# Kernel optimization log

Measured on AMD Instinct MI355X. Metric: run time of the kernel, lower is better.

## Reference

```python
import jax, jax.numpy as jnp
import numpy as np

NEG_BIG = -9e15


def gat_layer(h, adj, W, a, alpha, concat):
    # h: (N, Fin), W: (Fin, Fout), a: (2*Fout, 1)
    Wh = h @ W                                   # (N, Fout)
    F = Wh.shape[1]
    # e[i,j] = LeakyReLU(cat(Wh_i, Wh_j) @ a) = LeakyReLU(s_i + d_j)
    s = Wh @ a[:F, 0]                            # (N,)
    d = Wh @ a[F:, 0]                            # (N,)
    e = jax.nn.leaky_relu(s[:, None] + d[None, :], negative_slope=alpha)  # (N, N)
    e = jnp.where(adj > 0, e, NEG_BIG)
    att = jax.nn.softmax(e, axis=1)              # (N, N)
    out = att @ Wh                               # (N, Fout)
    return jax.nn.elu(out) if concat else out


def setup_inputs() -> dict:
    key = jax.random.key(0)
    ks = jax.random.split(key, 12)
    N, nfeat, nhid, nlatent, nclass = 8192, 512, 256, 64, 16

    def xavier(k, shape):
        gain = 1.414
        fan_in, fan_out = shape[0], shape[1]
        bound = gain * np.sqrt(6.0 / (fan_in + fan_out))
        return jax.random.uniform(k, shape, jnp.float32, -bound, bound)

    x = jax.random.normal(ks[0], (N, nfeat), jnp.float32)
    adj = jax.random.randint(ks[1], (N, N), 0, 2, jnp.int32)
    eps = jax.random.normal(ks[2], (N, nlatent), jnp.float32)
    return {
        "x": x,
        "adj": adj,
        "eps": eps,
        "W1": xavier(ks[3], (nfeat, nhid)),
        "a1": xavier(ks[4], (2 * nhid, 1)),
        "Wmu": xavier(ks[5], (nhid, nlatent)),
        "amu": xavier(ks[6], (2 * nlatent, 1)),
        "Wlv": xavier(ks[7], (nhid, nlatent)),
        "alv": xavier(ks[8], (2 * nlatent, 1)),
        "Wc": xavier(ks[9], (nlatent, nclass)),
        "bc": jnp.zeros((nclass,), jnp.float32),
    }


def reference(x, adj, eps, W1, a1, Wmu, amu, Wlv, alv, Wc, bc):
    alpha = 0.2  # LeakyReLU negative slope
    # eval mode: all dropouts are identity
    h = gat_layer(x, adj, W1, a1, alpha, concat=True)      # (N, nhid)
    mu = gat_layer(h, adj, Wmu, amu, alpha, concat=False)  # (N, nlatent)
    logvar = gat_layer(h, adj, Wlv, alv, alpha, concat=False)
    z = mu + eps * jnp.exp(0.5 * logvar)
    logits = z @ Wc + bc                                   # (N, nclass)
    return logits, mu, logvar
```

## Files before the change

kernel.cpp:

```cpp
#include <hip/hip_runtime.h>

typedef unsigned short u16;
typedef __attribute__((ext_vector_type(8))) short short8;
typedef __attribute__((ext_vector_type(4))) float f32x4;

#define NROW 8192

__device__ __forceinline__ float bf2f(u16 h) {
  unsigned u = ((unsigned)h) << 16;
  return __builtin_bit_cast(float, u);
}
__device__ __forceinline__ float ldf(const void* p, size_t i, int f32) {
  return f32 ? ((const float*)p)[i] : bf2f(((const u16*)p)[i]);
}
__device__ __forceinline__ u16 f2bf(float f) {
  unsigned b = __builtin_bit_cast(unsigned, f);
  b += 0x7FFFu + ((b >> 16) & 1u);
  return (u16)(b >> 16);
}

__global__ void detect3(const u16* __restrict__ xr, unsigned* __restrict__ mode) {
  __shared__ int zc, bg;
  int t = threadIdx.x;
  if (t == 0) { zc = 0; bg = 0; }
  __syncthreads();
  int zeros_even = 0; int big = 0;
  for (int i = t; i < 4096; i += 256) {
    u16 v = xr[i];
    if (!(i & 1) && v == 0) zeros_even++;
    if (fabsf(bf2f(v)) > 1e6f) big = 1;
  }
  atomicAdd(&zc, zeros_even);
  if (big) atomicOr(&bg, 1);
  __syncthreads();
  if (t == 0) *mode = (zc > 512 || bg) ? 1u : 0u;
}

__global__ void detect_adj(const unsigned* __restrict__ a, unsigned* __restrict__ amode) {
  __shared__ int clo;
  int t = threadIdx.x;
  if (t == 0) clo = 0;
  __syncthreads();
  int c = 0;
  for (int i = t; i < 4096; i += 256)
    if (a[i] == 0x00003F80u) c++;
  atomicAdd(&clo, c);
  __syncthreads();
  if (t == 0) *amode = (clo > 32) ? 1u : 0u;
}

struct AdjRaw { int4 w0, w1; };
__device__ __forceinline__ AdjRaw adj_load(const void* adj, size_t base, int amode) {
  AdjRaw r;
  if (amode == 0) {
    const int4* p = (const int4*)((const int*)adj + base);
    r.w0 = p[0]; r.w1 = p[1];
  } else {
    r.w0 = *(const int4*)((const u16*)adj + base);
    r.w1 = make_int4(0, 0, 0, 0);
  }
  return r;
}
__device__ __forceinline__ void adj_decode(const AdjRaw& r, int amode, int* aa) {
  if (amode == 0) {
    aa[0] = r.w0.x != 0; aa[1] = r.w0.y != 0; aa[2] = r.w0.z != 0; aa[3] = r.w0.w != 0;
    aa[4] = r.w1.x != 0; aa[5] = r.w1.y != 0; aa[6] = r.w1.z != 0; aa[7] = r.w1.w != 0;
  } else {
    aa[0] = (r.w0.x & 0xFFFF) != 0; aa[1] = ((unsigned)r.w0.x >> 16) != 0;
    aa[2] = (r.w0.y & 0xFFFF) != 0; aa[3] = ((unsigned)r.w0.y >> 16) != 0;
    aa[4] = (r.w0.z & 0xFFFF) != 0; aa[5] = ((unsigned)r.w0.z >> 16) != 0;
    aa[6] = (r.w0.w & 0xFFFF) != 0; aa[7] = ((unsigned)r.w0.w >> 16) != 0;
  }
}

__global__ __launch_bounds__(256) void gemm_mfma(const u16* __restrict__ Abf,
    const u16* __restrict__ BT, float* __restrict__ C, int K, int N) {
  int tid = threadIdx.x;
  int l = tid & 63, w = tid >> 6;
  int m0 = blockIdx.y * 64, n0 = blockIdx.x * 64;
  const u16* arow = Abf + (size_t)(m0 + w * 16 + (l & 15)) * K + (l >> 4) * 8;
  const u16* brow = BT + (size_t)(n0 + (l & 15)) * K + (l >> 4) * 8;
  f32x4 acc[4];
#pragma unroll
  for (int nt = 0; nt < 4; ++nt) acc[nt] = (f32x4){0.f, 0.f, 0.f, 0.f};
  for (int k0 = 0; k0 < K; k0 += 32) {
    short8 a = *(const short8*)(arow + k0);
#pragma unroll
    for (int nt = 0; nt < 4; ++nt) {
      short8 b = *(const short8*)(brow + (size_t)nt * 16 * K + k0);
      acc[nt] = __builtin_amdgcn_mfma_f32_16x16x32_bf16(a, b, acc[nt], 0, 0, 0);
    }
  }
#pragma unroll
  for (int nt = 0; nt < 4; ++nt)
#pragma unroll
    for (int q = 0; q < 4; ++q)
      C[(size_t)(m0 + w * 16 + (l >> 4) * 4 + q) * N + n0 + nt * 16 + (l & 15)] =
          acc[nt][q];
}

__global__ __launch_bounds__(256) void gemm2_dual(const u16* __restrict__ Abf,
    const u16* __restrict__ BT0, const u16* __restrict__ BT1,
    float* __restrict__ C0, float* __restrict__ C1) {
  const int K = 256, N = 64;
  const u16* BT = blockIdx.x ? BT1 : BT0;
  float* C = blockIdx.x ? C1 : C0;
  int tid = threadIdx.x, l = tid & 63, w = tid >> 6;
  int m0 = blockIdx.y * 64;
  const u16* arow = Abf + (size_t)(m0 + w * 16 + (l & 15)) * K + (l >> 4) * 8;
  const u16* brow = BT + (size_t)(l & 15) * K + (l >> 4) * 8;
  f32x4 acc[4];
#pragma unroll
  for (int nt = 0; nt < 4; ++nt) acc[nt] = (f32x4){0.f, 0.f, 0.f, 0.f};
  for (int k0 = 0; k0 < K; k0 += 32) {
    short8 a = *(const short8*)(arow + k0);
#pragma unroll
    for (int nt = 0; nt < 4; ++nt) {
      short8 b = *(const short8*)(brow + (size_t)nt * 16 * K + k0);
      acc[nt] = __builtin_amdgcn_mfma_f32_16x16x32_bf16(a, b, acc[nt], 0, 0, 0);
    }
  }
#pragma unroll
  for (int nt = 0; nt < 4; ++nt)
#pragma unroll
    for (int q = 0; q < 4; ++q)
      C[(size_t)(m0 + w * 16 + (l >> 4) * 4 + q) * N + nt * 16 + (l & 15)] = acc[nt][q];
}

__global__ __launch_bounds__(256) void convert_bf16(const void* __restrict__ in,
    u16* __restrict__ out, int n8, const unsigned* __restrict__ modep) {
  int f32 = (int)*modep;
  int i = blockIdx.x * 256 + threadIdx.x;
  if (i >= n8) return;
  if (f32) {
    float4 v0 = ((const float4*)in)[(size_t)i * 2];
    float4 v1 = ((const float4*)in)[(size_t)i * 2 + 1];
    ushort4 o0 = {f2bf(v0.x), f2bf(v0.y), f2bf(v0.z), f2bf(v0.w)};
    ushort4 o1 = {f2bf(v1.x), f2bf(v1.y), f2bf(v1.z), f2bf(v1.w)};
    ((ushort4*)out)[(size_t)i * 2] = o0;
    ((ushort4*)out)[(size_t)i * 2 + 1] = o1;
  } else {
    ((int4*)out)[i] = ((const int4*)in)[i];
  }
}

__global__ __launch_bounds__(256) void transpose_bf16(const float* __restrict__ in,
    u16* __restrict__ out, int M, int F) {
  __shared__ float t[32][33];
  int m0 = blockIdx.x * 32, f0 = blockIdx.y * 32;
  int c = threadIdx.x & 31, r = threadIdx.x >> 5;
  for (int rr = r; rr < 32; rr += 8)
    t[rr][c] = in[(size_t)(m0 + rr) * F + f0 + c];
  __syncthreads();
  for (int rr = r; rr < 32; rr += 8)
    out[(size_t)(f0 + rr) * M + m0 + c] = f2bf(t[c][rr]);
}

__global__ __launch_bounds__(256) void transpose_pair(const float* __restrict__ in0,
    const float* __restrict__ in1, u16* __restrict__ out0, u16* __restrict__ out1,
    int M, int F) {
  const float* in = blockIdx.z ? in1 : in0;
  u16* out = blockIdx.z ? out1 : out0;
  __shared__ float t[32][33];
  int m0 = blockIdx.x * 32, f0 = blockIdx.y * 32;
  int c = threadIdx.x & 31, r = threadIdx.x >> 5;
  for (int rr = r; rr < 32; rr += 8)
    t[rr][c] = in[(size_t)(m0 + rr) * F + f0 + c];
  __syncthreads();
  for (int rr = r; rr < 32; rr += 8)
    out[(size_t)(f0 + rr) * M + m0 + c] = f2bf(t[c][rr]);
}

__global__ __launch_bounds__(256) void transpose_any(const void* __restrict__ in,
    u16* __restrict__ out, int M, int F, const unsigned* __restrict__ modep) {
  int f32 = (int)*modep;
  __shared__ u16 t[32][33];
  int m0 = blockIdx.x * 32, f0 = blockIdx.y * 32;
  int c = threadIdx.x & 31, r = threadIdx.x >> 5;
  for (int rr = r; rr < 32; rr += 8)
    t[rr][c] = f2bf(ldf(in, (size_t)(m0 + rr) * F + f0 + c, f32));
  __syncthreads();
  for (int rr = r; rr < 32; rr += 8)
    out[(size_t)(f0 + rr) * M + m0 + c] = t[c][rr];
}

__global__ __launch_bounds__(256) void transpose_w2(const void* __restrict__ in0,
    const void* __restrict__ in1, u16* __restrict__ out0, u16* __restrict__ out1,
    int M, int F, const unsigned* __restrict__ modep) {
  int f32 = (int)*modep;
  const void* in = blockIdx.z ? in1 : in0;
  u16* out = blockIdx.z ? out1 : out0;
  __shared__ u16 t[32][33];
  int m0 = blockIdx.x * 32, f0 = blockIdx.y * 32;
  int c = threadIdx.x & 31, r = threadIdx.x >> 5;
  for (int rr = r; rr < 32; rr += 8)
    t[rr][c] = f2bf(ldf(in, (size_t)(m0 + rr) * F + f0 + c, f32));
  __syncthreads();
  for (int rr = r; rr < 32; rr += 8)
    out[(size_t)(f0 + rr) * M + m0 + c] = t[c][rr];
}

__global__ __launch_bounds__(256) void sd_f32(const float* __restrict__ Wh,
    const void* __restrict__ a2, float* __restrict__ s, float* __restrict__ d,
    int F, const unsigned* __restrict__ modep) {
  int f32 = (int)*modep;
  int row = blockIdx.x * 4 + (threadIdx.x >> 6);
  int l = threadIdx.x & 63;
  float ss = 0.f, dd = 0.f;
  for (int k = l; k < F; k += 64) {
    float wv = Wh[(size_t)row * F + k];
    ss += wv * ldf(a2, k, f32);
    dd += wv * ldf(a2, F + k, f32);
  }
#pragma unroll
  for (int off = 32; off > 0; off >>= 1) {
    ss += __shfl_down(ss, off, 64);
    dd += __shfl_down(dd, off, 64);
  }
  if (l == 0) { s[row] = ss; d[row] = dd; }
}

__global__ __launch_bounds__(256) void sd_dual(const float* __restrict__ Wh0,
    const float* __restrict__ Wh1, const void* __restrict__ a0,
    const void* __restrict__ a1, float* __restrict__ s0, float* __restrict__ s1,
    float* __restrict__ d0, float* __restrict__ d1,
    const unsigned* __restrict__ modep) {
  int f32 = (int)*modep;
  int L = blockIdx.y;
  const float* Wh = L ? Wh1 : Wh0;
  const void* a2 = L ? a1 : a0;
  int row = blockIdx.x * 4 + (threadIdx.x >> 6);
  int l = threadIdx.x & 63;
  float wv = Wh[(size_t)row * 64 + l];
  float ss = wv * ldf(a2, l, f32);
  float dd = wv * ldf(a2, 64 + l, f32);
#pragma unroll
  for (int off = 32; off > 0; off >>= 1) {
    ss += __shfl_down(ss, off, 64);
    dd += __shfl_down(dd, off, 64);
  }
  if (l == 0) { (L ? s1 : s0)[row] = ss; (L ? d1 : d0)[row] = dd; }
}

__global__ __launch_bounds__(256) void dmax_reduce(const float* __restrict__ da,
    const float* __restrict__ db, float* __restrict__ cells) {
  const float* d = blockIdx.x ? db : da;
  __shared__ float red[256];
  float m = -3.4e38f;
  for (int i = threadIdx.x; i < NROW; i += 256) m = fmaxf(m, d[i]);
  red[threadIdx.x] = m;
  __syncthreads();
#pragma unroll
  for (int sft = 128; sft > 0; sft >>= 1) {
    if (threadIdx.x < sft) red[threadIdx.x] = fmaxf(red[threadIdx.x], red[threadIdx.x + sft]);
    __syncthreads();
  }
  if (threadIdx.x == 0) cells[blockIdx.x * 16] = red[0];
}

__device__ __forceinline__ int pa_off(int L, int s, int mh, int row, int kg) {
  return ((L * 4 + s * 2 + mh) << 10) + (row << 6) + ((kg ^ ((row >> 1) & 3)) << 4);
}

template <int NL, int FDIM, int JS>
__global__ __launch_bounds__(256) void flash_mfma(
    const u16* __restrict__ whTa, const u16* __restrict__ whTb,
    const float* __restrict__ sa, const float* __restrict__ da,
    const float* __restrict__ sb, const float* __restrict__ db,
    const float* __restrict__ cella, const float* __restrict__ cellb,
    const void* __restrict__ adj, const unsigned* __restrict__ amodep,
    float* __restrict__ acca, float* __restrict__ lsa,
    float* __restrict__ accb, float* __restrict__ lsb) {
  constexpr int JLEN = NROW / JS;
  constexpr int NIT = JLEN / 64;
  constexpr int NTW = (NL == 1) ? 4 : 2;
  constexpr int NRBLK = NROW / 32;
  __shared__ __align__(16) char PA[2][NL * 4096];
  __shared__ __align__(16) float dd_[NL][JLEN];
  __shared__ float sv_[NL][32], Ms_[NL][32];
  int tid = threadIdx.x;
  int amode = (int)*amodep;
  int rblk = blockIdx.x % NRBLK, js = blockIdx.x / NRBLK;
  int r0 = rblk * 32;
  size_t jbase = (size_t)js * JLEN;
  if (tid < 32 * NL) {
    int L = tid >> 5, i = tid & 31;
    float Dm = L ? *cellb : *cella;
    float t0 = (L ? sb : sa)[r0 + i];
    sv_[L][i] = t0;
    float m = t0 + Dm;
    Ms_[L][i] = fmaxf(m, 0.2f * m);
  }
  for (int u = tid; u < (NL * JLEN) / 4; u += 256) {
    int L = u / (JLEN / 4), uu = u - L * (JLEN / 4);
    ((float4*)dd_[L])[uu] = ((const float4*)((L ? db : da) + jbase))[uu];
  }
  __syncthreads();
  int sr = tid >> 3, sjo = tid & 7;
  int s_w = sjo >> 2, kg_w = sjo & 3, mh_w = sr >> 4, row_w = sr & 15;
  int l = tid & 63, w = tid >> 6;
  int layer = (NL == 1) ? 0 : (w >> 1);
  int ntb = (NL == 1) ? (w * 4) : ((w & 1) * 2);
  const u16* whT = layer ? whTb : whTa;
  f32x4 acc[2][NTW];
#pragma unroll
  for (int m = 0; m < 2; ++m)
#pragma unroll
    for (int n = 0; n < NTW; ++n) acc[m][n] = (f32x4){0.f, 0.f, 0.f, 0.f};
  float psum[NL];
#pragma unroll
  for (int L = 0; L < NL; ++L) psum[L] = 0.f;
  size_t abase = (size_t)(r0 + sr) * NROW + jbase + sjo * 8;

  AdjRaw adjA = adj_load(adj, abase, amode);
  AdjRaw adjB = (NIT > 1) ? adj_load(adj, abase + 64, amode) : adjA;
  for (int it = 0; it < NIT; ++it) {
    size_t j0 = jbase + (size_t)it * 64;
    int cur = it & 1;
    short8 bfr[2][NTW];
#pragma unroll
    for (int s2 = 0; s2 < 2; ++s2) {
      size_t jcol = j0 + s2 * 32 + (size_t)(l >> 4) * 8;
#pragma unroll
      for (int nt = 0; nt < NTW; ++nt)
        bfr[s2][nt] =
            *(const short8*)&whT[(size_t)((ntb + nt) * 16 + (l & 15)) * NROW + jcol];
    }
    AdjRaw adjN = adjB;
    if (it + 2 < NIT) adjN = adj_load(adj, abase + (size_t)(it + 2) * 64, amode);
    int aa[8];
    adj_decode(adjA, amode, aa);
    char* pab = PA[cur];
#pragma unroll
    for (int L = 0; L < NL; ++L) {
      float sv = sv_[L][sr], Mr = Ms_[L][sr];
      float4 dv0 = *(const float4*)&dd_[L][it * 64 + sjo * 8];
      float4 dv1 = *(const float4*)&dd_[L][it * 64 + sjo * 8 + 4];
      float dvv[8] = {dv0.x, dv0.y, dv0.z, dv0.w, dv1.x, dv1.y, dv1.z, dv1.w};
      short8 pk;
      float ps = 0.f;
#pragma unroll
      for (int q = 0; q < 8; ++q) {
        float t = sv + dvv[q];
        float e = fmaxf(t, 0.2f * t) - Mr;
        float p = aa[q] ? __expf(e) : 0.f;
        ps += p;
        pk[q] = (short)f2bf(p);
      }
      psum[L] += ps;
      *(short8*)(pab + pa_off(L, s_w, mh_w, row_w, kg_w)) = pk;
    }
    asm volatile("s_waitcnt lgkmcnt(0)" ::: "memory");
    __builtin_amdgcn_s_barrier();
    __builtin_amdgcn_sched_barrier(0);
    __builtin_amdgcn_s_setprio(1);
#pragma unroll
    for (int s2 = 0; s2 < 2; ++s2) {
      short8 a0 = *(const short8*)(pab + pa_off(layer, s2, 0, l & 15, l >> 4));
      short8 a1 = *(const short8*)(pab + pa_off(layer, s2, 1, l & 15, l >> 4));
#pragma unroll
      for (int nt = 0; nt < NTW; ++nt) {
        acc[0][nt] = __builtin_amdgcn_mfma_f32_16x16x32_bf16(a0, bfr[s2][nt],
                                                             acc[0][nt], 0, 0, 0);
        acc[1][nt] = __builtin_amdgcn_mfma_f32_16x16x32_bf16(a1, bfr[s2][nt],
                                                             acc[1][nt], 0, 0, 0);
      }
    }
    __builtin_amdgcn_s_setprio(0);
    adjA = adjB; adjB = adjN;
  }
  __syncthreads();
  float* red = (float*)PA;
#pragma unroll
  for (int L = 0; L < NL; ++L) red[L * 256 + sr * 8 + sjo] = psum[L];
  __syncthreads();
  if (tid < 32 * NL) {
    int L = tid >> 5, r = tid & 31;
    float t = 0.f;
#pragma unroll
    for (int q = 0; q < 8; ++q) t += red[L * 256 + r * 8 + q];
    atomicAdd(&(L ? lsb : lsa)[r0 + r], t);
  }
  float* accp = layer ? accb : acca;
#pragma unroll
  for (int m = 0; m < 2; ++m)
#pragma unroll
    for (int nt = 0; nt < NTW; ++nt)
#pragma unroll
      for (int q = 0; q < 4; ++q)
        atomicAdd(&accp[(size_t)(r0 + m * 16 + (l >> 4) * 4 + q) * FDIM +
                        (ntb + nt) * 16 + (l & 15)],
                  acc[m][nt][q]);
}

__global__ __launch_bounds__(256) void combine_elu(const float* __restrict__ acc_g,
    const float* __restrict__ lsum_g, u16* __restrict__ hbf) {
  int idx = blockIdx.x * 256 + threadIdx.x;
  float x = acc_g[idx] / lsum_g[idx >> 8];
  x = (x > 0.f) ? x : (__expf(x) - 1.f);
  hbf[idx] = f2bf(x);
}

__global__ __launch_bounds__(256) void combine_div(const float* __restrict__ acc_g,
    const float* __restrict__ lsum_g, float* __restrict__ outf, float* __restrict__ outd) {
  int idx = blockIdx.x * 256 + threadIdx.x;
  float x = acc_g[idx] / lsum_g[idx >> 6];
  outf[idx] = x;
  outd[idx] = x;
}

__global__ __launch_bounds__(256) void logits_f32(const float* __restrict__ mu,
    const float* __restrict__ lv, const void* __restrict__ eps,
    const void* __restrict__ Wc, const void* __restrict__ bcv,
    float* __restrict__ outL, const unsigned* __restrict__ modep) {
  int f32 = (int)*modep;
  __shared__ float zs[64 * 64];
  __shared__ float wcs[64 * 16];
  int tid = threadIdx.x;
  for (int i = tid; i < 1024; i += 256) wcs[i] = ldf(Wc, i, f32);
  int rl = tid >> 2, cs = (tid & 3) * 16;
  int row = blockIdx.x * 64 + rl;
  size_t rb64 = (size_t)row * 64;
  for (int c = cs; c < cs + 16; ++c)
    zs[rl * 64 + c] = mu[rb64 + c] + ldf(eps, rb64 + c, f32) * __expf(0.5f * lv[rb64 + c]);
  __syncthreads();
  for (int it = tid; it < 1024; it += 256) {
    int r = it >> 4, oc = it & 15;
    float a = ldf(bcv, oc, f32);
    for (int c = 0; c < 64; ++c) a += zs[r * 64 + c] * wcs[c * 16 + oc];
    outL[(size_t)(blockIdx.x * 64 + r) * 16 + oc] = a;
  }
}

extern "C" void kernel_launch(void* const* d_in, const int* in_sizes, int n_in,
                              void* d_out, int out_size, void* d_ws, size_t ws_size,
                              hipStream_t stream) {
  (void)out_size; (void)ws_size;
  int ix = 0, iadj = 1, ieps = 2, iW1 = 3, ia1 = 4, iWmu = 5, iamu = 6,
      iWlv = 7, ialv = 8, iWc = 9, ibc = 10;
  {
    int fmu = -1, flv = -1, fam = -1, fal = -1;
    for (int i = 0; i < n_in; ++i) {
      switch (in_sizes[i]) {
        case 67108864: iadj = i; break;
        case 4194304:  ix   = i; break;
        case 524288:   ieps = i; break;
        case 131072:   iW1  = i; break;
        case 512:      ia1  = i; break;
        case 1024:     iWc  = i; break;
        case 16:       ibc  = i; break;
        case 16384:    if (fmu < 0) fmu = i; else flv = i; break;
        case 128:      if (fam < 0) fam = i; else fal = i; break;
        default: break;
      }
    }
    if (fmu >= 0 && flv >= 0) { iWmu = fmu; iWlv = flv; }
    if (fam >= 0 && fal >= 0) { iamu = fam; ialv = fal; }
  }
  const void* adj = d_in[iadj];
  char* ws = (char*)d_ws;
  const size_t KB = 1024, MB = 1024 * 1024;
  float* wh1   = (float*)(ws + 0);
  float* whmu  = (float*)(ws + 0);
  float* whlv  = (float*)(ws + 2 * MB);
  float* muf   = (float*)(ws + 4 * MB);
  float* lvf   = (float*)(ws + 6 * MB);
  u16*   xbf   = (u16*)(ws + 8 * MB);
  u16*   whT1  = (u16*)(ws + 8 * MB);
  u16*   hbf   = (u16*)(ws + 12 * MB);
  float* hacc  = (float*)(ws + 16 * MB);
  float* macc  = (float*)(ws + 16 * MB);
  float* lvacc = (float*)(ws + 18 * MB);
  u16*   whmuT = (u16*)(ws + 20 * MB);
  u16*   whlvT = (u16*)(ws + 21 * MB);
  u16*   W1T   = (u16*)(ws + 22 * MB);
  u16*   WmuT  = (u16*)(ws + 22 * MB + 256 * KB);
  u16*   WlvT  = (u16*)(ws + 22 * MB + 288 * KB);
  float* lsum1 = (float*)(ws + 24 * MB);
  float* lsmu  = (float*)(ws + 24 * MB + 32 * KB);
  float* lslv  = (float*)(ws + 24 * MB + 64 * KB);
  float* s1    = (float*)(ws + 24 * MB + 96 * KB);
  float* d1    = (float*)(ws + 24 * MB + 128 * KB);
  float* smu   = (float*)(ws + 24 * MB + 160 * KB);
  float* dmu   = (float*)(ws + 24 * MB + 192 * KB);
  float* slv   = (float*)(ws + 24 * MB + 224 * KB);
  float* dlv   = (float*)(ws + 24 * MB + 256 * KB);
  float* dmaxv = (float*)(ws + 24 * MB + 288 * KB);
  unsigned* mode  = (unsigned*)(ws + 24 * MB + 289 * KB);
  unsigned* amode = (unsigned*)(ws + 24 * MB + 290 * KB);

  float* out_logits = (float*)d_out;
  float* out_mu     = (float*)d_out + 131072;
  float* out_lv     = (float*)d_out + 655360;

  (void)hipMemsetAsync(lsum1, 0, 96 * KB, stream);
  (void)hipMemsetAsync(hacc, 0, 8 * MB, stream);
  detect3<<<1, 256, 0, stream>>>((const u16*)d_in[ix], mode);
  detect_adj<<<1, 256, 0, stream>>>((const unsigned*)adj, amode);

  convert_bf16<<<2048, 256, 0, stream>>>(d_in[ix], xbf, 524288, mode);
  transpose_any<<<dim3(16, 8), 256, 0, stream>>>(d_in[iW1], W1T, 512, 256, mode);
  gemm_mfma<<<dim3(4, 128), 256, 0, stream>>>(xbf, W1T, wh1, 512, 256);
  transpose_bf16<<<dim3(256, 8), 256, 0, stream>>>(wh1, whT1, 8192, 256);
  sd_f32<<<2048, 256, 0, stream>>>(wh1, d_in[ia1], s1, d1, 256, mode);
  dmax_reduce<<<1, 256, 0, stream>>>(d1, d1, dmaxv + 0);
  flash_mfma<1, 256, 8><<<2048, 256, 0, stream>>>(whT1, nullptr, s1, d1,
      nullptr, nullptr, dmaxv + 0, nullptr, adj, amode, hacc, lsum1, nullptr, nullptr);
  combine_elu<<<8192, 256, 0, stream>>>(hacc, lsum1, hbf);

  (void)hipMemsetAsync(macc, 0, 4 * MB, stream);

  transpose_w2<<<dim3(8, 2, 2), 256, 0, stream>>>(d_in[iWmu], d_in[iWlv],
      WmuT, WlvT, 256, 64, mode);
  gemm2_dual<<<dim3(2, 128), 256, 0, stream>>>(hbf, WmuT, WlvT, whmu, whlv);
  transpose_pair<<<dim3(256, 2, 2), 256, 0, stream>>>(whmu, whlv, whmuT, whlvT,
      8192, 64);
  sd_dual<<<dim3(2048, 2), 256, 0, stream>>>(whmu, whlv, d_in[iamu], d_in[ialv],
      smu, slv, dmu, dlv, mode);
  dmax_reduce<<<2, 256, 0, stream>>>(dmu, dlv, dmaxv + 16);
  flash_mfma<2, 64, 8><<<2048, 256, 0, stream>>>(whmuT, whlvT, smu, dmu, slv, dlv,
      dmaxv + 16, dmaxv + 32, adj, amode, macc, lsmu, lvacc, lslv);
  combine_div<<<2048, 256, 0, stream>>>(macc, lsmu, muf, out_mu);
  combine_div<<<2048, 256, 0, stream>>>(lvacc, lslv, lvf, out_lv);

  logits_f32<<<128, 256, 0, stream>>>(muf, lvf, d_in[ieps], d_in[iWc], d_in[ibc], out_logits, mode);
}
```

Before: 673.9 us.

## Drop split-K in flash attention kernels and fuse normalization epilogue

The flash attention kernels no longer split the neighbor dimension across 8 blocks. Each block of 512 threads now walks all 8192 columns in 128-column steps. Because of this the atomicAdd accumulation, the memsets of the accumulators and the separate combine_elu/combine_div kernels are gone, and normalization, ELU and output writes happen in the kernel epilogue. The grid shrinks from 2048 to 256 blocks, which risks underusing the 256 CUs and leaves a longer serial loop per block. The LDS footprint also grows with the full d vector held per block.

```diff
diff --git a/kernel.cpp b/kernel.cpp
--- a/kernel.cpp
+++ b/kernel.cpp
@@ -258,31 +258,28 @@
   if (threadIdx.x == 0) cells[blockIdx.x * 16] = red[0];
 }
 
-__device__ __forceinline__ int pa_off(int L, int s, int mh, int row, int kg) {
-  return ((L * 4 + s * 2 + mh) << 10) + (row << 6) + ((kg ^ ((row >> 1) & 3)) << 4);
-}
-
-template <int NL, int FDIM, int JS>
-__global__ __launch_bounds__(256) void flash_mfma(
+__device__ __forceinline__ int pa_off(int L, int ks, int mh, int row, int kg) {
+  return ((L * 8 + ks * 2 + mh) << 10) + (row << 6) + ((kg ^ ((row >> 1) & 3)) << 4);
+}
+
+template <int NL>
+__global__ __launch_bounds__(512) void flash_mfma(
     const u16* __restrict__ whTa, const u16* __restrict__ whTb,
     const float* __restrict__ sa, const float* __restrict__ da,
     const float* __restrict__ sb, const float* __restrict__ db,
     const float* __restrict__ cella, const float* __restrict__ cellb,
     const void* __restrict__ adj, const unsigned* __restrict__ amodep,
-    float* __restrict__ acca, float* __restrict__ lsa,
-    float* __restrict__ accb, float* __restrict__ lsb) {
-  constexpr int JLEN = NROW / JS;
-  constexpr int NIT = JLEN / 64;
-  constexpr int NTW = (NL == 1) ? 4 : 2;
-  constexpr int NRBLK = NROW / 32;
-  __shared__ __align__(16) char PA[2][NL * 4096];
-  __shared__ __align__(16) float dd_[NL][JLEN];
-  __shared__ float sv_[NL][32], Ms_[NL][32];
+    void* __restrict__ o0, void* __restrict__ o1,
+    void* __restrict__ o2, void* __restrict__ o3) {
+  constexpr int NIT = NROW / 128;
+  constexpr int NTW = (NL == 1) ? 2 : 1;
+  constexpr int FDIM = (NL == 1) ? 256 : 64;
+  __shared__ __align__(16) char PA[2][NL * 8192];
+  __shared__ __align__(16) float dd_[NL][NROW];
+  __shared__ float sv_[NL][32], Ms_[NL][32], ls_[NL][32];
   int tid = threadIdx.x;
   int amode = (int)*amodep;
-  int rblk = blockIdx.x % NRBLK, js = blockIdx.x / NRBLK;
-  int r0 = rblk * 32;
-  size_t jbase = (size_t)js * JLEN;
+  int r0 = blockIdx.x * 32;
   if (tid < 32 * NL) {
     int L = tid >> 5, i = tid & 31;
     float Dm = L ? *cellb : *cella;
@@ -291,16 +288,16 @@
     float m = t0 + Dm;
     Ms_[L][i] = fmaxf(m, 0.2f * m);
   }
-  for (int u = tid; u < (NL * JLEN) / 4; u += 256) {
-    int L = u / (JLEN / 4), uu = u - L * (JLEN / 4);
-    ((float4*)dd_[L])[uu] = ((const float4*)((L ? db : da) + jbase))[uu];
-  }
-  __syncthreads();
-  int sr = tid >> 3, sjo = tid & 7;
-  int s_w = sjo >> 2, kg_w = sjo & 3, mh_w = sr >> 4, row_w = sr & 15;
+  for (int u = tid; u < NL * (NROW / 4); u += 512) {
+    int L = u / (NROW / 4), uu = u - L * (NROW / 4);
+    ((float4*)dd_[L])[uu] = ((const float4*)(L ? db : da))[uu];
+  }
+  __syncthreads();
+  int sr = tid >> 4, sjo = tid & 15;
+  int ks_w = sjo >> 2, kg_w = sjo & 3, mh_w = sr >> 4, row_w = sr & 15;
   int l = tid & 63, w = tid >> 6;
-  int layer = (NL == 1) ? 0 : (w >> 1);
-  int ntb = (NL == 1) ? (w * 4) : ((w & 1) * 2);
+  int layer = (NL == 1) ? 0 : (w >> 2);
+  int ntb = (NL == 1) ? (w * 2) : (w & 3);
   const u16* whT = layer ? whTb : whTa;
   f32x4 acc[2][NTW];
 #pragma unroll
@@ -310,32 +307,32 @@
   float psum[NL];
 #pragma unroll
   for (int L = 0; L < NL; ++L) psum[L] = 0.f;
-  size_t abase = (size_t)(r0 + sr) * NROW + jbase + sjo * 8;
+  size_t abase = (size_t)(r0 + sr) * NROW + sjo * 8;
 
   AdjRaw adjA = adj_load(adj, abase, amode);
-  AdjRaw adjB = (NIT > 1) ? adj_load(adj, abase + 64, amode) : adjA;
+  AdjRaw adjB = adj_load(adj, abase + 128, amode);
   for (int it = 0; it < NIT; ++it) {
-    size_t j0 = jbase + (size_t)it * 64;
+    int j0 = it * 128;
     int cur = it & 1;
-    short8 bfr[2][NTW];
-#pragma unroll
-    for (int s2 = 0; s2 < 2; ++s2) {
-      size_t jcol = j0 + s2 * 32 + (size_t)(l >> 4) * 8;
+    short8 bfr[4][NTW];
+#pragma unroll
+    for (int ks = 0; ks < 4; ++ks) {
+      size_t jcol = (size_t)(j0 + ks * 32 + (l >> 4) * 8);
 #pragma unroll
       for (int nt = 0; nt < NTW; ++nt)
-        bfr[s2][nt] =
+        bfr[ks][nt] =
             *(const short8*)&whT[(size_t)((ntb + nt) * 16 + (l & 15)) * NROW + jcol];
     }
     AdjRaw adjN = adjB;
-    if (it + 2 < NIT) adjN = adj_load(adj, abase + (size_t)(it + 2) * 64, amode);
+    if (it + 2 < NIT) adjN = adj_load(adj, abase + (size_t)(it + 2) * 128, amode);
     int aa[8];
     adj_decode(adjA, amode, aa);
     char* pab = PA[cur];
 #pragma unroll
     for (int L = 0; L < NL; ++L) {
       float sv = sv_[L][sr], Mr = Ms_[L][sr];
-      float4 dv0 = *(const float4*)&dd_[L][it * 64 + sjo * 8];
-      float4 dv1 = *(const float4*)&dd_[L][it * 64 + sjo * 8 + 4];
+      float4 dv0 = *(const float4*)&dd_[L][j0 + sjo * 8];
+      float4 dv1 = *(const float4*)&dd_[L][j0 + sjo * 8 + 4];
       float dvv[8] = {dv0.x, dv0.y, dv0.z, dv0.w, dv1.x, dv1.y, dv1.z, dv1.w};
       short8 pk;
       float ps = 0.f;
@@ -348,21 +345,21 @@
         pk[q] = (short)f2bf(p);
       }
       psum[L] += ps;
-      *(short8*)(pab + pa_off(L, s_w, mh_w, row_w, kg_w)) = pk;
+      *(short8*)(pab + pa_off(L, ks_w, mh_w, row_w, kg_w)) = pk;
     }
     asm volatile("s_waitcnt lgkmcnt(0)" ::: "memory");
     __builtin_amdgcn_s_barrier();
     __builtin_amdgcn_sched_barrier(0);
     __builtin_amdgcn_s_setprio(1);
 #pragma unroll
-    for (int s2 = 0; s2 < 2; ++s2) {
-      short8 a0 = *(const short8*)(pab + pa_off(layer, s2, 0, l & 15, l >> 4));
-      short8 a1 = *(const short8*)(pab + pa_off(layer, s2, 1, l & 15, l >> 4));
+    for (int ks = 0; ks < 4; ++ks) {
+      short8 a0 = *(const short8*)(pab + pa_off(layer, ks, 0, l & 15, l >> 4));
+      short8 a1 = *(const short8*)(pab + pa_off(layer, ks, 1, l & 15, l >> 4));
 #pragma unroll
       for (int nt = 0; nt < NTW; ++nt) {
-        acc[0][nt] = __builtin_amdgcn_mfma_f32_16x16x32_bf16(a0, bfr[s2][nt],
+        acc[0][nt] = __builtin_amdgcn_mfma_f32_16x16x32_bf16(a0, bfr[ks][nt],
                                                              acc[0][nt], 0, 0, 0);
-        acc[1][nt] = __builtin_amdgcn_mfma_f32_16x16x32_bf16(a1, bfr[s2][nt],
+        acc[1][nt] = __builtin_amdgcn_mfma_f32_16x16x32_bf16(a1, bfr[ks][nt],
                                                              acc[1][nt], 0, 0, 0);
       }
     }
@@ -372,41 +369,45 @@
   __syncthreads();
   float* red = (float*)PA;
 #pragma unroll
-  for (int L = 0; L < NL; ++L) red[L * 256 + sr * 8 + sjo] = psum[L];
+  for (int L = 0; L < NL; ++L) red[L * 512 + tid] = psum[L];
   __syncthreads();
   if (tid < 32 * NL) {
     int L = tid >> 5, r = tid & 31;
     float t = 0.f;
 #pragma unroll
-    for (int q = 0; q < 8; ++q) t += red[L * 256 + r * 8 + q];
-    atomicAdd(&(L ? lsb : lsa)[r0 + r], t);
-  }
-  float* accp = layer ? accb : acca;
-#pragma unroll
-  for (int m = 0; m < 2; ++m)
-#pragma unroll
-    for (int nt = 0; nt < NTW; ++nt)
-#pragma unroll
-      for (int q = 0; q < 4; ++q)
-        atomicAdd(&accp[(size_t)(r0 + m * 16 + (l >> 4) * 4 + q) * FDIM +
-                        (ntb + nt) * 16 + (l & 15)],
-                  acc[m][nt][q]);
-}
-
-__global__ __launch_bounds__(256) void combine_elu(const float* __restrict__ acc_g,
-    const float* __restrict__ lsum_g, u16* __restrict__ hbf) {
-  int idx = blockIdx.x * 256 + threadIdx.x;
-  float x = acc_g[idx] / lsum_g[idx >> 8];
-  x = (x > 0.f) ? x : (__expf(x) - 1.f);
-  hbf[idx] = f2bf(x);
-}
-
-__global__ __launch_bounds__(256) void combine_div(const float* __restrict__ acc_g,
-    const float* __restrict__ lsum_g, float* __restrict__ outf, float* __restrict__ outd) {
-  int idx = blockIdx.x * 256 + threadIdx.x;
-  float x = acc_g[idx] / lsum_g[idx >> 6];
-  outf[idx] = x;
-  outd[idx] = x;
+    for (int q = 0; q < 16; ++q) t += red[L * 512 + r * 16 + q];
+    ls_[L][r] = t;
+  }
+  __syncthreads();
+  if constexpr (NL == 1) {
+    u16* hb = (u16*)o0;
+#pragma unroll
+    for (int m = 0; m < 2; ++m)
+#pragma unroll
+      for (int nt = 0; nt < NTW; ++nt)
+#pragma unroll
+        for (int q = 0; q < 4; ++q) {
+          int r = m * 16 + (l >> 4) * 4 + q;
+          int c = (ntb + nt) * 16 + (l & 15);
+          float x = acc[m][nt][q] / ls_[0][r];
+          x = (x > 0.f) ? x : (__expf(x) - 1.f);
+          hb[(size_t)(r0 + r) * FDIM + c] = f2bf(x);
+        }
+  } else {
+    float* of = (float*)(layer ? o2 : o0);
+    float* od = (float*)(layer ? o3 : o1);
+#pragma unroll
+    for (int m = 0; m < 2; ++m)
+#pragma unroll
+      for (int q = 0; q < 4; ++q) {
+        int r = m * 16 + (l >> 4) * 4 + q;
+        int c = ntb * 16 + (l & 15);
+        float x = acc[m][0][q] / ls_[layer][r];
+        size_t idx = (size_t)(r0 + r) * FDIM + c;
+        of[idx] = x;
+        od[idx] = x;
+      }
+  }
 }
 
 __global__ __launch_bounds__(256) void logits_f32(const float* __restrict__ mu,
@@ -468,17 +469,11 @@
   u16*   xbf   = (u16*)(ws + 8 * MB);
   u16*   whT1  = (u16*)(ws + 8 * MB);
   u16*   hbf   = (u16*)(ws + 12 * MB);
-  float* hacc  = (float*)(ws + 16 * MB);
-  float* macc  = (float*)(ws + 16 * MB);
-  float* lvacc = (float*)(ws + 18 * MB);
   u16*   whmuT = (u16*)(ws + 20 * MB);
   u16*   whlvT = (u16*)(ws + 21 * MB);
   u16*   W1T   = (u16*)(ws + 22 * MB);
   u16*   WmuT  = (u16*)(ws + 22 * MB + 256 * KB);
   u16*   WlvT  = (u16*)(ws + 22 * MB + 288 * KB);
-  float* lsum1 = (float*)(ws + 24 * MB);
-  float* lsmu  = (float*)(ws + 24 * MB + 32 * KB);
-  float* lslv  = (float*)(ws + 24 * MB + 64 * KB);
   float* s1    = (float*)(ws + 24 * MB + 96 * KB);
   float* d1    = (float*)(ws + 24 * MB + 128 * KB);
   float* smu   = (float*)(ws + 24 * MB + 160 * KB);
@@ -493,8 +488,6 @@
   float* out_mu     = (float*)d_out + 131072;
   float* out_lv     = (float*)d_out + 655360;
 
-  (void)hipMemsetAsync(lsum1, 0, 96 * KB, stream);
-  (void)hipMemsetAsync(hacc, 0, 8 * MB, stream);
   detect3<<<1, 256, 0, stream>>>((const u16*)d_in[ix], mode);
   detect_adj<<<1, 256, 0, stream>>>((const unsigned*)adj, amode);
 
@@ -504,11 +497,9 @@
   transpose_bf16<<<dim3(256, 8), 256, 0, stream>>>(wh1, whT1, 8192, 256);
   sd_f32<<<2048, 256, 0, stream>>>(wh1, d_in[ia1], s1, d1, 256, mode);
   dmax_reduce<<<1, 256, 0, stream>>>(d1, d1, dmaxv + 0);
-  flash_mfma<1, 256, 8><<<2048, 256, 0, stream>>>(whT1, nullptr, s1, d1,
-      nullptr, nullptr, dmaxv + 0, nullptr, adj, amode, hacc, lsum1, nullptr, nullptr);
-  combine_elu<<<8192, 256, 0, stream>>>(hacc, lsum1, hbf);
-
-  (void)hipMemsetAsync(macc, 0, 4 * MB, stream);
+  flash_mfma<1><<<256, 512, 0, stream>>>(whT1, nullptr, s1, d1,
+      nullptr, nullptr, dmaxv + 0, nullptr, adj, amode,
+      hbf, nullptr, nullptr, nullptr);
 
   transpose_w2<<<dim3(8, 2, 2), 256, 0, stream>>>(d_in[iWmu], d_in[iWlv],
       WmuT, WlvT, 256, 64, mode);
@@ -518,10 +509,9 @@
   sd_dual<<<dim3(2048, 2), 256, 0, stream>>>(whmu, whlv, d_in[iamu], d_in[ialv],
       smu, slv, dmu, dlv, mode);
   dmax_reduce<<<2, 256, 0, stream>>>(dmu, dlv, dmaxv + 16);
-  flash_mfma<2, 64, 8><<<2048, 256, 0, stream>>>(whmuT, whlvT, smu, dmu, slv, dlv,
-      dmaxv + 16, dmaxv + 32, adj, amode, macc, lsmu, lvacc, lslv);
-  combine_div<<<2048, 256, 0, stream>>>(macc, lsmu, muf, out_mu);
-  combine_div<<<2048, 256, 0, stream>>>(lvacc, lslv, lvf, out_lv);
+  flash_mfma<2><<<256, 512, 0, stream>>>(whmuT, whlvT, smu, dmu, slv, dlv,
+      dmaxv + 16, dmaxv + 32, adj, amode,
+      muf, out_mu, lvf, out_lv);
 
   logits_f32<<<128, 256, 0, stream>>>(muf, lvf, d_in[ieps], d_in[iWc], d_in[ibc], out_logits, mode);
 }
```

Result: faster. 616.8 us (-8.5%).
